# Optimization experiments

Measured on AMD Instinct MI355X. Metric: run time of the kernel, lower is better.

The kernel has to match this reference:

```python
import jax, jax.numpy as jnp
import numpy as np

EPS = 1e-5


def conv1x1(x, w, b):
    # x: [B,Cin,H,W], w: [Cout,Cin], b: [Cout]
    return jnp.einsum('oc,bchw->bohw', w, x) + b[None, :, None, None]


def fourier_unit(x, w, b, gamma, beta):
    # Replicates FourierUnit: fft2 -> keep half-spectrum -> conv1x1+BN(train)+ReLU
    # -> explicit Hermitian reconstruction (as written, incl. col-0 overwrite) -> ifft2.real
    Wd = x.shape[-1]
    Wf = Wd // 2 + 1
    y = jnp.fft.rfft2(x)  # == fft2(x)[..., :Wf] for real x; [B,C,H,Wf]
    yc = jnp.concatenate([y.real, y.imag], axis=1)  # [B,2C,H,Wf]
    yc = conv1x1(yc, w, b)
    mu = yc.mean(axis=(0, 2, 3), keepdims=True)
    var = yc.var(axis=(0, 2, 3), keepdims=True)  # biased, matches torch BN normalization
    yc = (yc - mu) * jax.lax.rsqrt(var + EPS) * gamma[None, :, None, None] + beta[None, :, None, None]
    yc = jax.nn.relu(yc)
    yr, yi = jnp.split(yc, 2, axis=1)
    h1 = jax.lax.complex(yr, yi)  # [B,C,H,Wf]
    # hr[r] = h1[(H-r) % H] along the H axis
    hr = jnp.roll(h1[:, :, ::-1, :], 1, axis=2)
    # Column layout of the manually-built 'hermitian' array of width (Wf-1)*2 = Wd:
    #   col 0        -> conj(hr[..., 0])        (overwritten by the nested loop)
    #   cols 1..Wf-1 -> h1[..., 1:Wf]           (untouched, incl. Nyquist col)
    #   cols Wf..W-1 -> conj(hr[..., W-c]) = conj(flip(hr[..., 1:Wf-1]))
    full = jnp.concatenate(
        [jnp.conj(hr[..., 0:1]), h1[..., 1:], jnp.conj(hr[..., 1:Wf - 1][..., ::-1])],
        axis=-1,
    )
    return jnp.fft.ifft2(full).real  # [B,C,H,Wd]


def local_fourier_unit(x, w, b, gamma, beta):
    # 2x2 spatial chunk -> channel concat -> FourierUnit -> 2x2 tile
    y5, y6 = jnp.split(x, 2, axis=2)
    y1, y2 = jnp.split(y5, 2, axis=3)
    y3, y4 = jnp.split(y6, 2, axis=3)
    y = jnp.concatenate([y1, y2, y3, y4], axis=1)
    y = fourier_unit(y, w, b, gamma, beta)
    y = jnp.concatenate([y, y], axis=2)
    return jnp.concatenate([y, y], axis=3)


def setup_inputs() -> dict:
    key = jax.random.key(0)
    ks = jax.random.split(key, 16)
    B, C, H, W = 4, 128, 256, 256
    Cg = C // 2          # 64 (ceil(0.5*C))
    Cl = C - Cg          # 64
    Ci = Cg // 2         # 32
    s = 0.05
    inp = {
        'x': jax.random.normal(ks[0], (B, C, H, W), jnp.float32),
        'w_local': jax.random.normal(ks[1], (Cl, Cl), jnp.float32) * s,
        'b_local': jax.random.normal(ks[2], (Cl,), jnp.float32) * s,
        'w_in': jax.random.normal(ks[3], (Ci, Cg), jnp.float32) * s,
        'b_in': jax.random.normal(ks[4], (Ci,), jnp.float32) * s,
        'w_out': jax.random.normal(ks[5], (Cg, Ci), jnp.float32) * s,
        'b_out': jax.random.normal(ks[6], (Cg,), jnp.float32) * s,
        'w_g2l': jax.random.normal(ks[7], (Cl, Cg), jnp.float32) * s,
        'b_g2l': jax.random.normal(ks[8], (Cl,), jnp.float32) * s,
        'w_l2g': jax.random.normal(ks[9], (Cg, Cl), jnp.float32) * s,
        'b_l2g': jax.random.normal(ks[10], (Cg,), jnp.float32) * s,
        'w_fu1': jax.random.normal(ks[11], (2 * Ci, 2 * Ci), jnp.float32) * s,
        'b_fu1': jax.random.normal(ks[12], (2 * Ci,), jnp.float32) * s,
        'g_fu1': jnp.ones((2 * Ci,), jnp.float32),
        'be_fu1': jnp.zeros((2 * Ci,), jnp.float32),
        'w_fu2': jax.random.normal(ks[13], (2 * Ci, 2 * Ci), jnp.float32) * s,
        'b_fu2': jax.random.normal(ks[14], (2 * Ci,), jnp.float32) * s,
        'g_fu2': jnp.ones((2 * Ci,), jnp.float32),
        'be_fu2': jnp.zeros((2 * Ci,), jnp.float32),
    }
    return inp


def reference(x, w_local, b_local, w_in, b_in, w_out, b_out,
              w_g2l, b_g2l, w_l2g, b_l2g,
              w_fu1, b_fu1, g_fu1, be_fu1,
              w_fu2, b_fu2, g_fu2, be_fu2):
    C = x.shape[1]
    Cg = -(-C // 2)  # ceil((1 - 0.5) * C)
    x_g = x[:, :Cg]
    x_l = x[:, Cg:]
    # Local path
    Y_ll = conv1x1(x_l, w_local, b_local)
    # Global transform path
    y_in = conv1x1(x_g, w_in, b_in)                       # [B, Cg/2, H, W]
    y_g = fourier_unit(y_in, w_fu1, b_fu1, g_fu1, be_fu1)
    Ci = y_in.shape[1]
    y_sg = y_in[:, 3 * (Ci // 4):]                        # last quarter of channels
    y_sg = local_fourier_unit(y_sg, w_fu2, b_fu2, g_fu2, be_fu2)
    Y_gg = conv1x1(y_sg + y_g, w_out, b_out)
    # Cross paths
    g2l = conv1x1(x_g, w_g2l, b_g2l)
    l2g = conv1x1(x_l, w_l2g, b_l2g)
    Y_l = Y_ll + g2l
    Y_g = Y_gg + l2g
    return jnp.concatenate([Y_g, Y_l], axis=1)
```

## Files before the change

### kernel.cpp

```cpp
#include <hip/hip_runtime.h>
#include <math.h>


#define PI2 6.283185307179586f

__device__ __forceinline__ void fma4(float4& a, float w, const float4& v) {
  a.x += w * v.x; a.y += w * v.y; a.z += w * v.z; a.w += w * v.w;
}
__device__ __forceinline__ float4 add4(const float4& a, const float4& b) {
  return make_float4(a.x + b.x, a.y + b.y, a.z + b.z, a.w + b.w);
}

template<int N, int LOG2N>
__device__ __forceinline__ void fft_stages(float* re, float* im, int tid, float sign) {
#pragma unroll
  for (int s = 1; s <= LOG2N; ++s) {
    __syncthreads();
    const int half = 1 << (s - 1);
    const int j = tid & (half - 1);
    const int i1 = ((tid >> (s - 1)) << s) + j;
    const int i2 = i1 + half;
    float ang = sign * (PI2 / (float)(1 << s)) * (float)j;
    float wr, wi;
    __sincosf(ang, &wi, &wr);
    float xr = re[i2], xi = im[i2];
    float vr = xr * wr - xi * wi;
    float vi = xr * wi + xi * wr;
    float ur = re[i1], ui = im[i1];
    re[i1] = ur + vr; im[i1] = ui + vi;
    re[i2] = ur - vr; im[i2] = ui - vi;
  }
  __syncthreads();
}

__global__ void rfft_fused(const float* __restrict__ y_in,
                           float2* __restrict__ S1, float2* __restrict__ S2) {
  __shared__ float re[256], im[256];
  const int t = threadIdx.x;
  if (blockIdx.x < 32768) {
    const int row = blockIdx.x;
    const float* p = y_in + (size_t)row * 256;
    for (int i = t; i < 256; i += 128) {
      int j = __brev((unsigned)i) >> 24;
      re[j] = p[i];
      im[j] = 0.f;
    }
    fft_stages<256, 8>(re, im, t, -1.f);
    float2* q = S1 + (size_t)row * 129;
    for (int k = t; k <= 128; k += 128) q[k] = make_float2(re[k], im[k]);
  } else {
    const int sub = t >> 6, t64 = t & 63;
    const int row = (blockIdx.x - 32768) * 2 + sub;
    const int h2 = row & 127;
    const int c2 = (row >> 7) & 31;
    const int b  = row >> 12;
    const int q = c2 >> 3, ch = c2 & 7;
    const int hs = ((q >> 1) << 7) + h2;
    const int ws0 = (q & 1) << 7;
    const float* p = y_in + (((size_t)(b * 32 + 24 + ch) * 256 + hs) * 256 + ws0);
    float* r = &re[sub * 128];
    float* iv = &im[sub * 128];
    for (int i = t64; i < 128; i += 64) {
      int j = __brev((unsigned)i) >> 25;
      r[j] = p[i];
      iv[j] = 0.f;
    }
    fft_stages<128, 7>(r, iv, t64, -1.f);
    float2* qp = S2 + (size_t)row * 65;
    for (int k = t64; k <= 64; k += 64) qp[k] = make_float2(r[k], iv[k]);
  }
}

template<int N, int LOG2N>
__device__ __forceinline__ void cfft_cols_body(float2* __restrict__ data, int Wf, float sign,
                                               int tilesPerImg, int bid,
                                               float* __restrict__ re, float* __restrict__ im) {
  const int TW = 16;
  const int img = bid / tilesPerImg;
  const int k0 = (bid % tilesPerImg) * TW;
  const int cols = min(TW, Wf - k0);
  float2* base = data + (size_t)img * N * Wf + k0;
  const int t = threadIdx.x;
  const int c = t & (TW - 1);
  const int g = t >> 4;
  const bool act = (c < cols);
  for (int r = g; r < N; r += 16) {
    float2 v;
    if (act) v = base[(size_t)r * Wf + c];
    int j = __brev((unsigned)r) >> (32 - LOG2N);
    if (act) { re[j * 17 + c] = v.x; im[j * 17 + c] = v.y; }
  }
#pragma unroll
  for (int s = 1; s <= LOG2N; ++s) {
    __syncthreads();
    const int half = 1 << (s - 1);
    for (int bf = g; bf < N / 2; bf += 16) {
      if (!act) continue;
      const int j = bf & (half - 1);
      const int i1 = ((bf >> (s - 1)) << s) + j;
      const int i2 = i1 + half;
      float ang = sign * (PI2 / (float)(1 << s)) * (float)j;
      float wr, wi;
      __sincosf(ang, &wi, &wr);
      float xr = re[i2 * 17 + c], xi = im[i2 * 17 + c];
      float vr = xr * wr - xi * wi;
      float vi = xr * wi + xi * wr;
      float ur = re[i1 * 17 + c], ui = im[i1 * 17 + c];
      re[i1 * 17 + c] = ur + vr; im[i1 * 17 + c] = ui + vi;
      re[i2 * 17 + c] = ur - vr; im[i2 * 17 + c] = ui - vi;
    }
  }
  __syncthreads();
  for (int r = g; r < N; r += 16) {
    if (act) base[(size_t)r * Wf + c] = make_float2(re[r * 17 + c], im[r * 17 + c]);
  }
}

__global__ void cfft_cols_fused(float2* __restrict__ d1, float2* __restrict__ d2) {
  __shared__ float re[256 * 17], im[256 * 17];
  if (blockIdx.x < 1152)
    cfft_cols_body<256, 8>(d1, 129, -1.f, 9, blockIdx.x, re, im);
  else
    cfft_cols_body<128, 7>(d2, 65, -1.f, 5, blockIdx.x - 1152, re, im);
}

template<int N, int LOG2N>
__device__ __forceinline__ void cfft_inv_body(const float* __restrict__ Z,
                            const float* __restrict__ scale, const float* __restrict__ shift,
                            float2* __restrict__ T, int Wf, int tilesPerImg, int chs, int bid,
                            float* __restrict__ re, float* __restrict__ im) {
  const int TW = 16;
  const int img = bid / tilesPerImg;
  const int b = img >> 5, cc = img & 31;
  const int k0 = (bid % tilesPerImg) * TW;
  const int cols = min(TW, Wf - k0);
  const int t = threadIdx.x;
  const int c = t & (TW - 1);
  const int g = t >> 4;
  const bool act = (c < cols);
  const int kk = k0 + c;
  const float scr = scale[cc], sfr = shift[cc];
  const float sci = scale[cc + 32], sfi = shift[cc + 32];
  const float* Zr = Z + (size_t)cc * chs + (size_t)b * N * Wf;
  const float* Zi = Z + (size_t)(cc + 32) * chs + (size_t)b * N * Wf;
  const bool edge = (kk == 0 || kk == Wf - 1);
  for (int r = g; r < N; r += 16) {
    float vr = 0.f, vi = 0.f;
    if (act) {
      size_t p = (size_t)r * Wf + kk;
      float yr = fmaxf(Zr[p] * scr + sfr, 0.f);
      float yi = fmaxf(Zi[p] * sci + sfi, 0.f);
      if (edge) {
        int rm = (N - r) & (N - 1);
        size_t pm = (size_t)rm * Wf + kk;
        float yr2 = fmaxf(Zr[pm] * scr + sfr, 0.f);
        float yi2 = fmaxf(Zi[pm] * sci + sfi, 0.f);
        yr = 0.5f * (yr + yr2);
        yi = 0.5f * (yi - yi2);
      }
      vr = yr; vi = yi;
    }
    int j = __brev((unsigned)r) >> (32 - LOG2N);
    if (act) { re[j * 17 + c] = vr; im[j * 17 + c] = vi; }
  }
#pragma unroll
  for (int s = 1; s <= LOG2N; ++s) {
    __syncthreads();
    const int half = 1 << (s - 1);
    for (int bf = g; bf < N / 2; bf += 16) {
      if (!act) continue;
      const int jq = bf & (half - 1);
      const int i1 = ((bf >> (s - 1)) << s) + jq;
      const int i2 = i1 + half;
      float ang = (PI2 / (float)(1 << s)) * (float)jq;
      float wr, wi;
      __sincosf(ang, &wi, &wr);
      float xr = re[i2 * 17 + c], xi = im[i2 * 17 + c];
      float pr = xr * wr - xi * wi;
      float pi = xr * wi + xi * wr;
      float ur = re[i1 * 17 + c], ui = im[i1 * 17 + c];
      re[i1 * 17 + c] = ur + pr; im[i1 * 17 + c] = ui + pi;
      re[i2 * 17 + c] = ur - pr; im[i2 * 17 + c] = ui - pi;
    }
  }
  __syncthreads();
  float2* base = T + (size_t)img * N * Wf + k0;
  for (int r = g; r < N; r += 16)
    if (act) base[(size_t)r * Wf + c] = make_float2(re[r * 17 + c], im[r * 17 + c]);
}

__global__ void cfft_inv_fused(const float* __restrict__ Z1, const float* __restrict__ st1,
                               float2* __restrict__ T1,
                               const float* __restrict__ Z2, const float* __restrict__ st2,
                               float2* __restrict__ T2) {
  __shared__ float re[256 * 17], im[256 * 17];
  if (blockIdx.x < 1152)
    cfft_inv_body<256, 8>(Z1, st1, st1 + 64, T1, 129, 9, 132096, blockIdx.x, re, im);
  else
    cfft_inv_body<128, 7>(Z2, st2, st2 + 64, T2, 65, 5, 33280, blockIdx.x - 1152, re, im);
}

__global__ void irfft_fused(const float2* __restrict__ T1, float* __restrict__ y_g,
                            const float2* __restrict__ T2, float* __restrict__ y2) {
  __shared__ float re[256], im[256];
  const int t = threadIdx.x;
  if (blockIdx.x < 32768) {
    const int row = blockIdx.x;
    const float2* p = T1 + (size_t)row * 129;
    for (int i = t; i < 256; i += 128) {
      float2 v;
      if (i <= 128) v = p[i];
      else { v = p[256 - i]; v.y = -v.y; }
      int j = __brev((unsigned)i) >> 24;
      re[j] = v.x; im[j] = v.y;
    }
    fft_stages<256, 8>(re, im, t, 1.f);
    float* q = y_g + (size_t)row * 256;
    for (int i = t; i < 256; i += 128) q[i] = re[i] * (1.f / 65536.f);
  } else {
    const int sub = t >> 6, t64 = t & 63;
    const int row = (blockIdx.x - 32768) * 2 + sub;
    const float2* p = T2 + (size_t)row * 65;
    float* r = &re[sub * 128];
    float* iv = &im[sub * 128];
    for (int i = t64; i < 128; i += 64) {
      float2 v;
      if (i <= 64) v = p[i];
      else { v = p[128 - i]; v.y = -v.y; }
      int j = __brev((unsigned)i) >> 25;
      r[j] = v.x; iv[j] = v.y;
    }
    fft_stages<128, 7>(r, iv, t64, 1.f);
    float* q = y2 + (size_t)row * 128;
    for (int i = t64; i < 128; i += 64) q[i] = r[i] * (1.f / 16384.f);
  }
}

__global__ __launch_bounds__(256, 4) void conv_in_v(const float* __restrict__ x,
                          const float* __restrict__ w,
                          const float* __restrict__ bias, float* __restrict__ y) {
  __shared__ float wt[32 * 64];
  __shared__ float bl[32];
  const int t = threadIdx.x;
  for (int idx = t; idx < 2048; idx += 256) wt[idx] = w[(idx & 31) * 64 + (idx >> 5)];
  if (t < 32) bl[t] = bias[t];
  __syncthreads();
  const int og = t >> 6;
  const int p4 = blockIdx.x * 64 + (t & 63);
  const int hw4 = p4 & 16383;
  const int b = p4 >> 14;
  const float4* xb = (const float4*)x + (size_t)b * 128 * 16384 + hw4;
  float4 acc[8];
#pragma unroll
  for (int o = 0; o < 8; ++o) { float bv = bl[og * 8 + o]; acc[o] = make_float4(bv, bv, bv, bv); }
  float4 n0 = xb[0], n1 = xb[16384], n2 = xb[2 * 16384], n3 = xb[3 * 16384];
  for (int ci = 0; ci < 64; ci += 4) {
    float4 c0 = n0, c1 = n1, c2 = n2, c3 = n3;
    if (ci < 60) {
      const float4* np = xb + (size_t)(ci + 4) * 16384;
      n0 = np[0]; n1 = np[16384]; n2 = np[2 * 16384]; n3 = np[3 * 16384];
    }
#pragma unroll
    for (int k = 0; k < 4; ++k) {
      float4 v = (k == 0) ? c0 : (k == 1) ? c1 : (k == 2) ? c2 : c3;
      const float4* w4p = (const float4*)&wt[(ci + k) * 32 + og * 8];
      float4 a = w4p[0], c = w4p[1];
      fma4(acc[0], a.x, v); fma4(acc[1], a.y, v); fma4(acc[2], a.z, v); fma4(acc[3], a.w, v);
      fma4(acc[4], c.x, v); fma4(acc[5], c.y, v); fma4(acc[6], c.z, v); fma4(acc[7], c.w, v);
    }
  }
  float4* yb = (float4*)y + (size_t)(b * 32 + og * 8) * 16384 + hw4;
#pragma unroll
  for (int o = 0; o < 8; ++o) yb[(size_t)o * 16384] = acc[o];
}

template<int B_, int H_, int Wf_>
__device__ __forceinline__ void conv_spec_body(const float4* __restrict__ S4,
                            const float* __restrict__ w, const float* __restrict__ bias,
                            float2* __restrict__ Z2, int bid, float* wt, float* bl) {
  constexpr int PP = H_ * Wf_ / 2;
  constexpr int CHS2 = B_ * PP;
  const int t = threadIdx.x;
  for (int idx = t; idx < 4096; idx += 256) wt[idx] = w[(idx & 63) * 64 + (idx >> 6)];
  if (t < 64) bl[t] = bias[t];
  __syncthreads();
  const int og = t >> 7;
  const int j2 = bid * 128 + (t & 127);
  const int b = j2 / PP;
  const int jp = j2 - b * PP;
  float2 acc[32];
#pragma unroll
  for (int o = 0; o < 32; ++o) { float bv = bl[og * 32 + o]; acc[o] = make_float2(bv, bv); }
  const float4* sp = S4 + (size_t)(b * 32) * PP + jp;
  float4 nv = sp[0];
  for (int ci = 0; ci < 32; ++ci) {
    float4 sv = nv;
    if (ci < 31) nv = sp[(size_t)(ci + 1) * PP];
    const float4* wr4 = (const float4*)&wt[ci * 64 + og * 32];
    const float4* wi4 = (const float4*)&wt[(ci + 32) * 64 + og * 32];
#pragma unroll
    for (int o4 = 0; o4 < 8; ++o4) {
      float4 a = wr4[o4], c = wi4[o4];
      acc[4 * o4 + 0].x += a.x * sv.x + c.x * sv.y;  acc[4 * o4 + 0].y += a.x * sv.z + c.x * sv.w;
      acc[4 * o4 + 1].x += a.y * sv.x + c.y * sv.y;  acc[4 * o4 + 1].y += a.y * sv.z + c.y * sv.w;
      acc[4 * o4 + 2].x += a.z * sv.x + c.z * sv.y;  acc[4 * o4 + 2].y += a.z * sv.z + c.z * sv.w;
      acc[4 * o4 + 3].x += a.w * sv.x + c.w * sv.y;  acc[4 * o4 + 3].y += a.w * sv.z + c.w * sv.w;
    }
  }
#pragma unroll
  for (int o = 0; o < 32; ++o) Z2[(size_t)(og * 32 + o) * CHS2 + j2] = acc[o];
}

__global__ __launch_bounds__(256, 4) void conv_spec_fused(
    const float4* __restrict__ S1, const float* __restrict__ w1, const float* __restrict__ b1,
    float2* __restrict__ Z1,
    const float4* __restrict__ S2, const float* __restrict__ w2, const float* __restrict__ b2,
    float2* __restrict__ Z2) {
  __shared__ float wt[4096];
  __shared__ float bl[64];
  if (blockIdx.x < 516)
    conv_spec_body<4, 256, 129>(S1, w1, b1, Z1, blockIdx.x, wt, bl);
  else
    conv_spec_body<4, 128, 65>(S2, w2, b2, Z2, blockIdx.x - 516, wt, bl);
}

__global__ void bn_stats_fused(const float* __restrict__ Z1, const float* __restrict__ Z2,
                               double* __restrict__ pb1, double* __restrict__ pb2) {
  int bid = blockIdx.x;
  const float* Z; double* pb; int chunk;
  if (bid < 2048) { Z = Z1; pb = pb1; chunk = 4128; }
  else { bid -= 2048; Z = Z2; pb = pb2; chunk = 1040; }
  const int c = bid >> 5;
  const int sl = bid & 31;
  const float* p = Z + (size_t)c * ((size_t)chunk * 32) + (size_t)sl * chunk;
  double s = 0.0, s2 = 0.0;
  for (int i = threadIdx.x; i < chunk; i += 256) {
    float v = p[i];
    s += v;
    s2 += (double)v * (double)v;
  }
  __shared__ double sh[256], sh2[256];
  sh[threadIdx.x] = s; sh2[threadIdx.x] = s2;
  __syncthreads();
  for (int off = 128; off > 0; off >>= 1) {
    if (threadIdx.x < off) { sh[threadIdx.x] += sh[threadIdx.x + off]; sh2[threadIdx.x] += sh2[threadIdx.x + off]; }
    __syncthreads();
  }
  if (threadIdx.x == 0) { pb[2 * bid] = sh[0]; pb[2 * bid + 1] = sh2[0]; }
}

__global__ void bn_finalize_fused(const double* __restrict__ pb1, const double* __restrict__ pb2,
                                  const float* __restrict__ g1, const float* __restrict__ be1,
                                  const float* __restrict__ g2, const float* __restrict__ be2,
                                  float* __restrict__ st1, float* __restrict__ st2) {
  const int t = threadIdx.x;
  const bool fu1 = (t < 64);
  const double* pb = fu1 ? pb1 : pb2;
  const int n = fu1 ? 132096 : 33280;
  const float* gamma = fu1 ? g1 : g2;
  const float* beta  = fu1 ? be1 : be2;
  float* scale = fu1 ? st1 : st2;
  float* shift = fu1 ? (st1 + 64) : (st2 + 64);
  const int c = t & 63;
  double s = 0.0, s2 = 0.0;
  for (int i = 0; i < 32; ++i) { s += pb[2 * (c * 32 + i)]; s2 += pb[2 * (c * 32 + i) + 1]; }
  double mu = s / (double)n;
  double var = s2 / (double)n - mu * mu;
  float rs = (float)(1.0 / sqrt(var + 1e-5));
  float g = gamma[c] * rs;
  scale[c] = g;
  shift[c] = beta[c] - (float)mu * g;
}

__device__ __forceinline__ void final_l_body(const float* __restrict__ x, float* __restrict__ out,
                                             const float* wg, const float* wl, const float* bb,
                                             int pblk, int t) {
  const int og = t >> 6;
  const int p4 = pblk * 64 + (t & 63);
  const int hw4 = p4 & 16383;
  const int b = p4 >> 14;
  const float4* xb = (const float4*)x + (size_t)b * 128 * 16384 + hw4;
  float4 acc[16];
#pragma unroll
  for (int o = 0; o < 16; ++o) { float bv = bb[og * 16 + o]; acc[o] = make_float4(bv, bv, bv, bv); }
  float4 g0 = xb[0], g1 = xb[16384];
  float4 l0 = xb[(size_t)64 * 16384], l1 = xb[(size_t)65 * 16384];
  for (int ci = 0; ci < 64; ci += 2) {
    float4 cg0 = g0, cg1 = g1, cl0 = l0, cl1 = l1;
    if (ci < 62) {
      const float4* np = xb + (size_t)(ci + 2) * 16384;
      g0 = np[0]; g1 = np[16384];
      l0 = np[(size_t)64 * 16384]; l1 = np[(size_t)65 * 16384];
    }
#pragma unroll
    for (int k = 0; k < 2; ++k) {
      float4 xg = k ? cg1 : cg0;
      float4 xl = k ? cl1 : cl0;
      const float4* g4 = (const float4*)&wg[(ci + k) * 64 + og * 16];
      const float4* l4 = (const float4*)&wl[(ci + k) * 64 + og * 16];
#pragma unroll
      for (int o4 = 0; o4 < 4; ++o4) {
        float4 a = g4[o4], cw = l4[o4];
        fma4(acc[4 * o4 + 0], a.x, xg); fma4(acc[4 * o4 + 0], cw.x, xl);
        fma4(acc[4 * o4 + 1], a.y, xg); fma4(acc[4 * o4 + 1], cw.y, xl);
        fma4(acc[4 * o4 + 2], a.z, xg); fma4(acc[4 * o4 + 2], cw.z, xl);
        fma4(acc[4 * o4 + 3], a.w, xg); fma4(acc[4 * o4 + 3], cw.w, xl);
      }
    }
  }
  float4* ob = (float4*)out + (size_t)(b * 128 + 64 + og * 16) * 16384 + hw4;
#pragma unroll
  for (int o = 0; o < 16; ++o) ob[(size_t)o * 16384] = acc[o];
}

__device__ __forceinline__ void final_g_body(const float* __restrict__ x,
                                             const float* __restrict__ y_g, const float* __restrict__ y2,
                                             float* __restrict__ out,
                                             const float* wo, const float* wl, const float* bb,
                                             int pblk, int t) {
  const int og = t >> 6;
  const int p4 = pblk * 64 + (t & 63);
  const int hw4 = p4 & 16383;
  const int b = p4 >> 14;
  const int h = hw4 >> 6;
  const int w4 = hw4 & 63;
  const int hw2_4 = ((h & 127) << 5) + (w4 & 31);
  const float4* xb = (const float4*)x + (size_t)(b * 128 + 64) * 16384 + hw4;
  const float4* gb = (const float4*)y_g + (size_t)b * 32 * 16384 + hw4;
  const float4* tb = (const float4*)y2 + (size_t)b * 32 * 4096 + hw2_4;
  float4 acc[16];
#pragma unroll
  for (int o = 0; o < 16; ++o) { float bv = bb[og * 16 + o]; acc[o] = make_float4(bv, bv, bv, bv); }
  float4 pg0 = gb[0], pg1 = gb[16384];
  float4 pt0 = tb[0], pt1 = tb[4096];
  for (int ci = 0; ci < 32; ci += 2) {
    float4 s0 = add4(pg0, pt0), s1 = add4(pg1, pt1);
    if (ci < 30) {
      const float4* gp = gb + (size_t)(ci + 2) * 16384;
      const float4* tp = tb + (size_t)(ci + 2) * 4096;
      pg0 = gp[0]; pg1 = gp[16384];
      pt0 = tp[0]; pt1 = tp[4096];
    }
#pragma unroll
    for (int k = 0; k < 2; ++k) {
      float4 s = k ? s1 : s0;
      const float4* w4p = (const float4*)&wo[(ci + k) * 64 + og * 16];
#pragma unroll
      for (int o4 = 0; o4 < 4; ++o4) {
        float4 a = w4p[o4];
        fma4(acc[4 * o4 + 0], a.x, s);
        fma4(acc[4 * o4 + 1], a.y, s);
        fma4(acc[4 * o4 + 2], a.z, s);
        fma4(acc[4 * o4 + 3], a.w, s);
      }
    }
  }
  float4 n0 = xb[0], n1 = xb[16384], n2 = xb[2 * 16384], n3 = xb[3 * 16384];
  for (int ci = 0; ci < 64; ci += 4) {
    float4 c0 = n0, c1 = n1, c2 = n2, c3 = n3;
    if (ci < 60) {
      const float4* np = xb + (size_t)(ci + 4) * 16384;
      n0 = np[0]; n1 = np[16384]; n2 = np[2 * 16384]; n3 = np[3 * 16384];
    }
#pragma unroll
    for (int k = 0; k < 4; ++k) {
      float4 xl = (k == 0) ? c0 : (k == 1) ? c1 : (k == 2) ? c2 : c3;
      const float4* w4p = (const float4*)&wl[(ci + k) * 64 + og * 16];
#pragma unroll
      for (int o4 = 0; o4 < 4; ++o4) {
        float4 a = w4p[o4];
        fma4(acc[4 * o4 + 0], a.x, xl);
        fma4(acc[4 * o4 + 1], a.y, xl);
        fma4(acc[4 * o4 + 2], a.z, xl);
        fma4(acc[4 * o4 + 3], a.w, xl);
      }
    }
  }
  float4* ob = (float4*)out + (size_t)(b * 128 + og * 16) * 16384 + hw4;
#pragma unroll
  for (int o = 0; o < 16; ++o) ob[(size_t)o * 16384] = acc[o];
}

__global__ __launch_bounds__(256, 4) void final_fused(const float* __restrict__ x,
                          const float* __restrict__ y_g, const float* __restrict__ y2,
                          const float* __restrict__ w_out, const float* __restrict__ b_out,
                          const float* __restrict__ w_l2g, const float* __restrict__ b_l2g,
                          const float* __restrict__ w_local, const float* __restrict__ b_local,
                          const float* __restrict__ w_g2l, const float* __restrict__ b_g2l,
                          float* __restrict__ out) {
  __shared__ float sA[64 * 64], sB[64 * 64], sbb[64];
  const int t = threadIdx.x;
  const int isL = blockIdx.x & 1;
  const int pblk = blockIdx.x >> 1;
  if (isL) {
    for (int idx = t; idx < 4096; idx += 256) {
      sA[idx] = w_g2l[(idx & 63) * 64 + (idx >> 6)];
      sB[idx] = w_local[(idx & 63) * 64 + (idx >> 6)];
    }
    if (t < 64) sbb[t] = b_local[t] + b_g2l[t];
    __syncthreads();
    final_l_body(x, out, sA, sB, sbb, pblk, t);
  } else {
    for (int idx = t; idx < 2048; idx += 256) sA[idx] = w_out[(idx & 63) * 32 + (idx >> 6)];
    for (int idx = t; idx < 4096; idx += 256) sB[idx] = w_l2g[(idx & 63) * 64 + (idx >> 6)];
    if (t < 64) sbb[t] = b_out[t] + b_l2g[t];
    __syncthreads();
    final_g_body(x, y_g, y2, out, sA, sB, sbb, pblk, t);
  }
}

extern "C" void kernel_launch(void* const* d_in, const int* in_sizes, int n_in,
                              void* d_out, int out_size, void* d_ws, size_t ws_size,
                              hipStream_t stream) {
  (void)in_sizes; (void)n_in; (void)out_size; (void)ws_size;
  const float* x       = (const float*)d_in[0];
  const float* w_local = (const float*)d_in[1];
  const float* b_local = (const float*)d_in[2];
  const float* w_in    = (const float*)d_in[3];
  const float* b_in    = (const float*)d_in[4];
  const float* w_out   = (const float*)d_in[5];
  const float* b_out   = (const float*)d_in[6];
  const float* w_g2l   = (const float*)d_in[7];
  const float* b_g2l   = (const float*)d_in[8];
  const float* w_l2g   = (const float*)d_in[9];
  const float* b_l2g   = (const float*)d_in[10];
  const float* w_fu1   = (const float*)d_in[11];
  const float* b_fu1   = (const float*)d_in[12];
  const float* g_fu1   = (const float*)d_in[13];
  const float* be_fu1  = (const float*)d_in[14];
  const float* w_fu2   = (const float*)d_in[15];
  const float* b_fu2   = (const float*)d_in[16];
  const float* g_fu2   = (const float*)d_in[17];
  const float* be_fu2  = (const float*)d_in[18];
  float* out = (float*)d_out;

  float* ws   = (float*)d_ws;
  float* y_in = ws;
  float* S1   = y_in + 8388608;
  float* Z1   = S1 + 8454144;
  float* y_g  = Z1;
  float* S2   = Z1 + 8454144;
  float* Z2   = S2 + 2129920;
  float* y2   = Z2;
  float* st1  = Z2 + 2129920;
  float* st2  = st1 + 128;
  double* pb1 = (double*)S1;
  double* pb2 = (double*)S2;

  conv_in_v<<<1024, 256, 0, stream>>>(x, w_in, b_in, y_in);

  rfft_fused<<<32768 + 8192, 128, 0, stream>>>(y_in, (float2*)S1, (float2*)S2);
  cfft_cols_fused<<<1152 + 640, 256, 0, stream>>>((float2*)S1, (float2*)S2);

  conv_spec_fused<<<516 + 130, 256, 0, stream>>>((const float4*)S1, w_fu1, b_fu1, (float2*)Z1,
                                                 (const float4*)S2, w_fu2, b_fu2, (float2*)Z2);
  bn_stats_fused<<<4096, 256, 0, stream>>>(Z1, Z2, pb1, pb2);
  bn_finalize_fused<<<1, 128, 0, stream>>>(pb1, pb2, g_fu1, be_fu1, g_fu2, be_fu2, st1, st2);

  cfft_inv_fused<<<1152 + 640, 256, 0, stream>>>(Z1, st1, (float2*)S1, Z2, st2, (float2*)S2);
  irfft_fused<<<32768 + 8192, 128, 0, stream>>>((const float2*)S1, y_g, (const float2*)S2, y2);

  final_fused<<<2048, 256, 0, stream>>>(x, y_g, y2, w_out, b_out, w_l2g, b_l2g,
                                        w_local, b_local, w_g2l, b_g2l, out);
}
```

Baseline: 583.0 us.

## Fuse BatchNorm statistics into spectral conv epilogue and finalize in inverse FFT

Each conv_spec thread now computes sum and sum-of-squares of its outputs, reduces them across the wavefront with shuffles, and atomically adds them to per-channel double accumulators. The inverse column FFT kernel derives scale and shift directly from those accumulators. This removes the separate bn_stats pass, which reread the full spectral tensor, and the bn_finalize launch. It adds a memset, per-output double shuffles and atomics in the conv epilogue, and a small redundant per-block finalize.

Result: slower. 838.4 us (+43.8%).

```diff
diff --git a/kernel.cpp b/kernel.cpp
--- a/kernel.cpp
+++ b/kernel.cpp
@@ -126,7 +126,8 @@
 
 template<int N, int LOG2N>
 __device__ __forceinline__ void cfft_inv_body(const float* __restrict__ Z,
-                            const float* __restrict__ scale, const float* __restrict__ shift,
+                            const double* __restrict__ pb, const float* __restrict__ gamma,
+                            const float* __restrict__ beta, float nInv,
                             float2* __restrict__ T, int Wf, int tilesPerImg, int chs, int bid,
                             float* __restrict__ re, float* __restrict__ im) {
   const int TW = 16;
@@ -139,8 +140,17 @@
   const int g = t >> 4;
   const bool act = (c < cols);
   const int kk = k0 + c;
-  const float scr = scale[cc], sfr = shift[cc];
-  const float sci = scale[cc + 32], sfi = shift[cc + 32];
+  const double n = 1.0 / (double)nInv;
+  double s_r = pb[2 * cc], q_r = pb[2 * cc + 1];
+  double s_i = pb[2 * (cc + 32)], q_i = pb[2 * (cc + 32) + 1];
+  double mu_r = s_r / n, var_r = q_r / n - mu_r * mu_r;
+  double mu_i = s_i / n, var_i = q_i / n - mu_i * mu_i;
+  float rs_r = (float)(1.0 / sqrt(var_r + 1e-5));
+  float rs_i = (float)(1.0 / sqrt(var_i + 1e-5));
+  const float scr = gamma[cc] * rs_r;
+  const float sfr = beta[cc] - (float)mu_r * scr;
+  const float sci = gamma[cc + 32] * rs_i;
+  const float sfi = beta[cc + 32] - (float)mu_i * sci;
   const float* Zr = Z + (size_t)cc * chs + (size_t)b * N * Wf;
   const float* Zi = Z + (size_t)(cc + 32) * chs + (size_t)b * N * Wf;
   const bool edge = (kk == 0 || kk == Wf - 1);
@@ -189,15 +199,17 @@
     if (act) base[(size_t)r * Wf + c] = make_float2(re[r * 17 + c], im[r * 17 + c]);
 }
 
-__global__ void cfft_inv_fused(const float* __restrict__ Z1, const float* __restrict__ st1,
+__global__ void cfft_inv_fused(const float* __restrict__ Z1, const double* __restrict__ pb1,
+                               const float* __restrict__ g1, const float* __restrict__ be1,
                                float2* __restrict__ T1,
-                               const float* __restrict__ Z2, const float* __restrict__ st2,
+                               const float* __restrict__ Z2, const double* __restrict__ pb2,
+                               const float* __restrict__ g2, const float* __restrict__ be2,
                                float2* __restrict__ T2) {
   __shared__ float re[256 * 17], im[256 * 17];
   if (blockIdx.x < 1152)
-    cfft_inv_body<256, 8>(Z1, st1, st1 + 64, T1, 129, 9, 132096, blockIdx.x, re, im);
+    cfft_inv_body<256, 8>(Z1, pb1, g1, be1, 1.f / 132096.f, T1, 129, 9, 132096, blockIdx.x, re, im);
   else
-    cfft_inv_body<128, 7>(Z2, st2, st2 + 64, T2, 65, 5, 33280, blockIdx.x - 1152, re, im);
+    cfft_inv_body<128, 7>(Z2, pb2, g2, be2, 1.f / 33280.f, T2, 65, 5, 33280, blockIdx.x - 1152, re, im);
 }
 
 __global__ void irfft_fused(const float2* __restrict__ T1, float* __restrict__ y_g,
@@ -277,7 +289,8 @@
 template<int B_, int H_, int Wf_>
 __device__ __forceinline__ void conv_spec_body(const float4* __restrict__ S4,
                             const float* __restrict__ w, const float* __restrict__ bias,
-                            float2* __restrict__ Z2, int bid, float* wt, float* bl) {
+                            float2* __restrict__ Z2, double* __restrict__ pb,
+                            int bid, float* wt, float* bl) {
   constexpr int PP = H_ * Wf_ / 2;
   constexpr int CHS2 = B_ * PP;
   const int t = threadIdx.x;
@@ -309,67 +322,31 @@
   }
 #pragma unroll
   for (int o = 0; o < 32; ++o) Z2[(size_t)(og * 32 + o) * CHS2 + j2] = acc[o];
+  for (int o = 0; o < 32; ++o) {
+    double s = (double)acc[o].x + (double)acc[o].y;
+    double q = (double)acc[o].x * (double)acc[o].x + (double)acc[o].y * (double)acc[o].y;
+    for (int off = 32; off > 0; off >>= 1) {
+      s += __shfl_down(s, off);
+      q += __shfl_down(q, off);
+    }
+    if ((t & 63) == 0) {
+      atomicAdd(&pb[2 * (og * 32 + o)], s);
+      atomicAdd(&pb[2 * (og * 32 + o) + 1], q);
+    }
+  }
 }
 
 __global__ __launch_bounds__(256, 4) void conv_spec_fused(
     const float4* __restrict__ S1, const float* __restrict__ w1, const float* __restrict__ b1,
-    float2* __restrict__ Z1,
+    float2* __restrict__ Z1, double* __restrict__ pb1,
     const float4* __restrict__ S2, const float* __restrict__ w2, const float* __restrict__ b2,
-    float2* __restrict__ Z2) {
+    float2* __restrict__ Z2, double* __restrict__ pb2) {
   __shared__ float wt[4096];
   __shared__ float bl[64];
   if (blockIdx.x < 516)
-    conv_spec_body<4, 256, 129>(S1, w1, b1, Z1, blockIdx.x, wt, bl);
+    conv_spec_body<4, 256, 129>(S1, w1, b1, Z1, pb1, blockIdx.x, wt, bl);
   else
-    conv_spec_body<4, 128, 65>(S2, w2, b2, Z2, blockIdx.x - 516, wt, bl);
-}
-
-__global__ void bn_stats_fused(const float* __restrict__ Z1, const float* __restrict__ Z2,
-                               double* __restrict__ pb1, double* __restrict__ pb2) {
-  int bid = blockIdx.x;
-  const float* Z; double* pb; int chunk;
-  if (bid < 2048) { Z = Z1; pb = pb1; chunk = 4128; }
-  else { bid -= 2048; Z = Z2; pb = pb2; chunk = 1040; }
-  const int c = bid >> 5;
-  const int sl = bid & 31;
-  const float* p = Z + (size_t)c * ((size_t)chunk * 32) + (size_t)sl * chunk;
-  double s = 0.0, s2 = 0.0;
-  for (int i = threadIdx.x; i < chunk; i += 256) {
-    float v = p[i];
-    s += v;
-    s2 += (double)v * (double)v;
-  }
-  __shared__ double sh[256], sh2[256];
-  sh[threadIdx.x] = s; sh2[threadIdx.x] = s2;
-  __syncthreads();
-  for (int off = 128; off > 0; off >>= 1) {
-    if (threadIdx.x < off) { sh[threadIdx.x] += sh[threadIdx.x + off]; sh2[threadIdx.x] += sh2[threadIdx.x + off]; }
-    __syncthreads();
-  }
-  if (threadIdx.x == 0) { pb[2 * bid] = sh[0]; pb[2 * bid + 1] = sh2[0]; }
-}
-
-__global__ void bn_finalize_fused(const double* __restrict__ pb1, const double* __restrict__ pb2,
-                                  const float* __restrict__ g1, const float* __restrict__ be1,
-                                  const float* __restrict__ g2, const float* __restrict__ be2,
-                                  float* __restrict__ st1, float* __restrict__ st2) {
-  const int t = threadIdx.x;
-  const bool fu1 = (t < 64);
-  const double* pb = fu1 ? pb1 : pb2;
-  const int n = fu1 ? 132096 : 33280;
-  const float* gamma = fu1 ? g1 : g2;
-  const float* beta  = fu1 ? be1 : be2;
-  float* scale = fu1 ? st1 : st2;
-  float* shift = fu1 ? (st1 + 64) : (st2 + 64);
-  const int c = t & 63;
-  double s = 0.0, s2 = 0.0;
-  for (int i = 0; i < 32; ++i) { s += pb[2 * (c * 32 + i)]; s2 += pb[2 * (c * 32 + i) + 1]; }
-  double mu = s / (double)n;
-  double var = s2 / (double)n - mu * mu;
-  float rs = (float)(1.0 / sqrt(var + 1e-5));
-  float g = gamma[c] * rs;
-  scale[c] = g;
-  shift[c] = beta[c] - (float)mu * g;
+    conv_spec_body<4, 128, 65>(S2, w2, b2, Z2, pb2, blockIdx.x - 516, wt, bl);
 }
 
 __device__ __forceinline__ void final_l_body(const float* __restrict__ x, float* __restrict__ out,
@@ -542,22 +519,21 @@
   float* S2   = Z1 + 8454144;
   float* Z2   = S2 + 2129920;
   float* y2   = Z2;
-  float* st1  = Z2 + 2129920;
-  float* st2  = st1 + 128;
-  double* pb1 = (double*)S1;
-  double* pb2 = (double*)S2;
+  double* pb1 = (double*)(Z2 + 2129920);
+  double* pb2 = pb1 + 128;
+
+  hipMemsetAsync(pb1, 0, 256 * sizeof(double), stream);
 
   conv_in_v<<<1024, 256, 0, stream>>>(x, w_in, b_in, y_in);
 
   rfft_fused<<<32768 + 8192, 128, 0, stream>>>(y_in, (float2*)S1, (float2*)S2);
   cfft_cols_fused<<<1152 + 640, 256, 0, stream>>>((float2*)S1, (float2*)S2);
 
-  conv_spec_fused<<<516 + 130, 256, 0, stream>>>((const float4*)S1, w_fu1, b_fu1, (float2*)Z1,
-                                                 (const float4*)S2, w_fu2, b_fu2, (float2*)Z2);
-  bn_stats_fused<<<4096, 256, 0, stream>>>(Z1, Z2, pb1, pb2);
-  bn_finalize_fused<<<1, 128, 0, stream>>>(pb1, pb2, g_fu1, be_fu1, g_fu2, be_fu2, st1, st2);
-
-  cfft_inv_fused<<<1152 + 640, 256, 0, stream>>>(Z1, st1, (float2*)S1, Z2, st2, (float2*)S2);
+  conv_spec_fused<<<516 + 130, 256, 0, stream>>>((const float4*)S1, w_fu1, b_fu1, (float2*)Z1, pb1,
+                                                 (const float4*)S2, w_fu2, b_fu2, (float2*)Z2, pb2);
+
+  cfft_inv_fused<<<1152 + 640, 256, 0, stream>>>(Z1, pb1, g_fu1, be_fu1, (float2*)S1,
+                                                 Z2, pb2, g_fu2, be_fu2, (float2*)S2);
   irfft_fused<<<32768 + 8192, 128, 0, stream>>>((const float2*)S1, y_g, (const float2*)S2, y2);
 
   final_fused<<<2048, 256, 0, stream>>>(x, y_g, y2, w_out, b_out, w_l2g, b_l2g,
```
